# Kernel optimization log

Measured on AMD Instinct MI355X. Metric: run time of the kernel, lower is better.

The kernel has to match this reference:

```python
import jax, jax.numpy as jnp
import numpy as np

K_SIZE = 3
SIGMA = 1.3


def _gauss_kernel():
    # Matches the original: K[y,x] = exp(-(x^2+y^2)/(2*sigma^2)), then normalized to sum 1.
    pad = K_SIZE // 2
    coords = jnp.arange(-pad, pad + 1, dtype=jnp.float32)
    g = jnp.exp(-(coords[:, None] ** 2 + coords[None, :] ** 2) / (2.0 * SIGMA ** 2))
    return g / g.sum()


def setup_inputs() -> dict:
    key = jax.random.key(0)
    im = jax.random.uniform(key, (1, 4096, 4096, 3), dtype=jnp.float32)  # non-negative photon-count-like image
    return {"im": im}


def reference(im):
    x = jnp.squeeze(im, 0)                       # [H, W, C]
    # Anscombe transform
    at = 2.0 * jnp.sqrt(x + 0.375)
    # 3x3 depthwise Gaussian blur with zero padding (pad=1), per channel
    C = at.shape[-1]
    kern = jnp.broadcast_to(_gauss_kernel()[:, :, None, None], (K_SIZE, K_SIZE, 1, C))
    y = jax.lax.conv_general_dilated(
        at[None], kern, window_strides=(1, 1), padding="SAME",
        dimension_numbers=("NHWC", "HWIO", "NHWC"), feature_group_count=C)[0]
    y = jnp.clip(y, 0.0, 255.0)
    # Inverse Anscombe transform (unbiased closed-form approximation)
    s = jnp.sqrt(jnp.float32(1.5))
    out = 0.25 * y ** 2 + 0.25 * s / y - (11.0 / 8.0) / (y ** 2) + 0.625 * s / (y ** 3) - 0.125
    return out
```

## Files before the change

kernel.cpp:

```cpp
#include <hip/hip_runtime.h>
#include <cmath>

constexpr int H   = 4096;
constexpr int W   = 4096;
constexpr int C   = 3;
constexpr int WF  = W * C;
constexpr int EPT = 8;
constexpr int TW  = 256 * EPT;
constexpr int RPT = 16;

typedef float f32x4 __attribute__((ext_vector_type(4)));

__device__ __forceinline__ float ans1(float v) {
    return 2.0f * __builtin_amdgcn_sqrtf(v + 0.375f);
}
__device__ __forceinline__ float4 ans4(float4 v) {
    return make_float4(ans1(v.x), ans1(v.y), ans1(v.z), ans1(v.w));
}

__global__ __launch_bounds__(256, 4) void anscombe_gauss_kernel(
    const float* __restrict__ in, float* __restrict__ out,
    float wa, float wb, float c1, float c3)
{
    const int tid = threadIdx.x;
    const int gc  = blockIdx.x * TW + tid * EPT;
    const int h0  = blockIdx.y * RPT;

    const bool okL = (gc >= 4);
    const bool okR = (gc + 12 <= WF);
    const int offL = okL ? gc - 4 : gc;
    const int offR = okR ? gc + 8 : gc;

    const float4 cfill = make_float4(-0.375f, -0.375f, -0.375f, -0.375f);

    auto loadrow = [&](int h, float4& lo, float4& hi, float4& hl, float4& hr) {
        if ((unsigned)h < (unsigned)H) {
            const float* rp = in + (long)h * WF;
            lo = *(const float4*)(rp + gc);
            hi = *(const float4*)(rp + gc + 4);
            hl = *(const float4*)(rp + offL);
            hr = *(const float4*)(rp + offR);
            if (!okL) hl = cfill;
            if (!okR) hr = cfill;
        } else {
            lo = hi = hl = hr = cfill;
        }
    };

    float4 pl, ph, pL, pR;
    loadrow(h0 - 1, pl, ph, pL, pR);

    float hp[8] = {0,0,0,0,0,0,0,0};
    float hc[8] = {0,0,0,0,0,0,0,0};

    #pragma unroll
    for (int s = 0; s < RPT + 2; ++s) {
        const float4 vlo = pl, vhi = ph, vhl = pL, vhr = pR;
        if (s < RPT + 1) loadrow(h0 + s, pl, ph, pL, pR);

        const float4 alo = ans4(vlo), ahi = ans4(vhi);
        const float m3 = ans1(vhl.y), m2 = ans1(vhl.z), m1 = ans1(vhl.w);
        const float p8 = ans1(vhr.x), p9 = ans1(vhr.y), pA = ans1(vhr.z);

        const float e0 = alo.x, e1 = alo.y, e2 = alo.z, e3 = alo.w;
        const float e4 = ahi.x, e5 = ahi.y, e6 = ahi.z, e7 = ahi.w;

        float hn[8];
        hn[0] = wa * (m3 + e3) + wb * e0;
        hn[1] = wa * (m2 + e4) + wb * e1;
        hn[2] = wa * (m1 + e5) + wb * e2;
        hn[3] = wa * (e0 + e6) + wb * e3;
        hn[4] = wa * (e1 + e7) + wb * e4;
        hn[5] = wa * (e2 + p8) + wb * e5;
        hn[6] = wa * (e3 + p9) + wb * e6;
        hn[7] = wa * (e4 + pA) + wb * e7;

        if (s >= 2) {
            const int ho = h0 + s - 2;
            float o[8];
            #pragma unroll
            for (int j = 0; j < 8; ++j) {
                float y = wa * (hp[j] + hn[j]) + wb * hc[j];
                y = fminf(fmaxf(y, 0.0f), 255.0f);
                float ry = __builtin_amdgcn_rcpf(y);
                o[j] = fmaf(0.25f * y, y,
                        fmaf(ry, fmaf(ry, fmaf(ry, c3, -1.375f), c1), -0.125f));
            }
            float* op = out + (long)ho * WF + gc;
            f32x4 o0 = {o[0], o[1], o[2], o[3]};
            f32x4 o1 = {o[4], o[5], o[6], o[7]};
            __builtin_nontemporal_store(o0, (f32x4*)op);
            __builtin_nontemporal_store(o1, (f32x4*)(op + 4));
        }
        #pragma unroll
        for (int j = 0; j < 8; ++j) { hp[j] = hc[j]; hc[j] = hn[j]; }
    }
}

extern "C" void kernel_launch(void* const* d_in, const int* in_sizes, int n_in,
                              void* d_out, int out_size, void* d_ws, size_t ws_size,
                              hipStream_t stream) {
    const float* in = (const float*)d_in[0];
    float* out      = (float*)d_out;

    const double sig2x2 = 2.0 * 1.3 * 1.3;
    const double e1     = std::exp(-1.0 / sig2x2);
    const double inv1d  = 1.0 / (1.0 + 2.0 * e1);
    const float  wa     = (float)(e1 * inv1d);
    const float  wb     = (float)inv1d;

    const double s  = std::sqrt(1.5);
    const float  c1 = (float)(0.25  * s);
    const float  c3 = (float)(0.625 * s);

    dim3 grid(WF / TW, H / RPT);
    anscombe_gauss_kernel<<<grid, 256, 0, stream>>>(in, out, wa, wb, c1, c3);
}
```

Baseline: 84.53 us.

## Fold Anscombe scale into blur weights, use med3 clamp, plain stores

After: 100.6 us. +19.0%, slower.

```diff
diff --git a/kernel.cpp b/kernel.cpp
--- a/kernel.cpp
+++ b/kernel.cpp
@@ -9,18 +9,16 @@
 constexpr int TW  = 256 * EPT;
 constexpr int RPT = 16;
 
-typedef float f32x4 __attribute__((ext_vector_type(4)));
-
-__device__ __forceinline__ float ans1(float v) {
-    return 2.0f * __builtin_amdgcn_sqrtf(v + 0.375f);
+__device__ __forceinline__ float sq1(float v) {
+    return __builtin_amdgcn_sqrtf(v + 0.375f);
 }
-__device__ __forceinline__ float4 ans4(float4 v) {
-    return make_float4(ans1(v.x), ans1(v.y), ans1(v.z), ans1(v.w));
+__device__ __forceinline__ float4 sq4(float4 v) {
+    return make_float4(sq1(v.x), sq1(v.y), sq1(v.z), sq1(v.w));
 }
 
 __global__ __launch_bounds__(256, 4) void anscombe_gauss_kernel(
     const float* __restrict__ in, float* __restrict__ out,
-    float wa, float wb, float c1, float c3)
+    float wa2, float wb2, float wa, float wb, float c1, float c3)
 {
     const int tid = threadIdx.x;
     const int gc  = blockIdx.x * TW + tid * EPT;
@@ -47,33 +45,33 @@
         }
     };
 
-    float4 pl, ph, pL, pR;
-    loadrow(h0 - 1, pl, ph, pL, pR);
+    float4 nlo, nhi, nhl, nhr;
+    loadrow(h0 - 1, nlo, nhi, nhl, nhr);
 
     float hp[8] = {0,0,0,0,0,0,0,0};
     float hc[8] = {0,0,0,0,0,0,0,0};
 
     #pragma unroll
     for (int s = 0; s < RPT + 2; ++s) {
-        const float4 vlo = pl, vhi = ph, vhl = pL, vhr = pR;
-        if (s < RPT + 1) loadrow(h0 + s, pl, ph, pL, pR);
+        const float4 vlo = nlo, vhi = nhi, vhl = nhl, vhr = nhr;
+        if (s < RPT + 1) loadrow(h0 + s, nlo, nhi, nhl, nhr);
 
-        const float4 alo = ans4(vlo), ahi = ans4(vhi);
-        const float m3 = ans1(vhl.y), m2 = ans1(vhl.z), m1 = ans1(vhl.w);
-        const float p8 = ans1(vhr.x), p9 = ans1(vhr.y), pA = ans1(vhr.z);
+        const float4 alo = sq4(vlo), ahi = sq4(vhi);
+        const float m3 = sq1(vhl.y), m2 = sq1(vhl.z), m1 = sq1(vhl.w);
+        const float p8 = sq1(vhr.x), p9 = sq1(vhr.y), pA = sq1(vhr.z);
 
         const float e0 = alo.x, e1 = alo.y, e2 = alo.z, e3 = alo.w;
         const float e4 = ahi.x, e5 = ahi.y, e6 = ahi.z, e7 = ahi.w;
 
         float hn[8];
-        hn[0] = wa * (m3 + e3) + wb * e0;
-        hn[1] = wa * (m2 + e4) + wb * e1;
-        hn[2] = wa * (m1 + e5) + wb * e2;
-        hn[3] = wa * (e0 + e6) + wb * e3;
-        hn[4] = wa * (e1 + e7) + wb * e4;
-        hn[5] = wa * (e2 + p8) + wb * e5;
-        hn[6] = wa * (e3 + p9) + wb * e6;
-        hn[7] = wa * (e4 + pA) + wb * e7;
+        hn[0] = wa2 * (m3 + e3) + wb2 * e0;
+        hn[1] = wa2 * (m2 + e4) + wb2 * e1;
+        hn[2] = wa2 * (m1 + e5) + wb2 * e2;
+        hn[3] = wa2 * (e0 + e6) + wb2 * e3;
+        hn[4] = wa2 * (e1 + e7) + wb2 * e4;
+        hn[5] = wa2 * (e2 + p8) + wb2 * e5;
+        hn[6] = wa2 * (e3 + p9) + wb2 * e6;
+        hn[7] = wa2 * (e4 + pA) + wb2 * e7;
 
         if (s >= 2) {
             const int ho = h0 + s - 2;
@@ -81,16 +79,14 @@
             #pragma unroll
             for (int j = 0; j < 8; ++j) {
                 float y = wa * (hp[j] + hn[j]) + wb * hc[j];
-                y = fminf(fmaxf(y, 0.0f), 255.0f);
+                y = __builtin_amdgcn_fmed3f(y, 0.0f, 255.0f);
                 float ry = __builtin_amdgcn_rcpf(y);
                 o[j] = fmaf(0.25f * y, y,
                         fmaf(ry, fmaf(ry, fmaf(ry, c3, -1.375f), c1), -0.125f));
             }
             float* op = out + (long)ho * WF + gc;
-            f32x4 o0 = {o[0], o[1], o[2], o[3]};
-            f32x4 o1 = {o[4], o[5], o[6], o[7]};
-            __builtin_nontemporal_store(o0, (f32x4*)op);
-            __builtin_nontemporal_store(o1, (f32x4*)(op + 4));
+            *(float4*)(op)     = make_float4(o[0], o[1], o[2], o[3]);
+            *(float4*)(op + 4) = make_float4(o[4], o[5], o[6], o[7]);
         }
         #pragma unroll
         for (int j = 0; j < 8; ++j) { hp[j] = hc[j]; hc[j] = hn[j]; }
@@ -108,11 +104,13 @@
     const double inv1d  = 1.0 / (1.0 + 2.0 * e1);
     const float  wa     = (float)(e1 * inv1d);
     const float  wb     = (float)inv1d;
+    const float  wa2    = (float)(2.0 * e1 * inv1d);
+    const float  wb2    = (float)(2.0 * inv1d);
 
     const double s  = std::sqrt(1.5);
     const float  c1 = (float)(0.25  * s);
     const float  c3 = (float)(0.625 * s);
 
     dim3 grid(WF / TW, H / RPT);
-    anscombe_gauss_kernel<<<grid, 256, 0, stream>>>(in, out, wa, wb, c1, c3);
+    anscombe_gauss_kernel<<<grid, 256, 0, stream>>>(in, out, wa2, wb2, wa, wb, c1, c3);
 }
```
